# Kernel optimization log

Hardware: AMD Instinct MI355X
Metric: run time of the kernel (lower is better)

## Reference

```python
import jax, jax.numpy as jnp
import numpy as np

N_NODES = 100000

def gcn_conv(x, W, b, row, col, n_nodes):
    """PyG-style GCNConv: add self-loops, symmetric deg normalization,
    linear transform, scatter-add aggregation over edges, plus bias."""
    h = x @ W  # [N, out]
    loop = jnp.arange(n_nodes, dtype=row.dtype)
    r = jnp.concatenate([row, loop])  # source nodes
    c = jnp.concatenate([col, loop])  # target nodes
    w = jnp.ones(r.shape[0], dtype=x.dtype)  # edge_weight=None -> ones (incl. self-loop fill=1)
    deg = jax.ops.segment_sum(w, c, num_segments=n_nodes)
    dinv = jnp.where(deg > 0, jax.lax.rsqrt(deg), 0.0).astype(x.dtype)
    norm = dinv[r] * dinv[c]  # [E+N]
    msg = h[r] * norm[:, None]  # gather + scale, [E+N, out]
    out = jax.ops.segment_sum(msg, c, num_segments=n_nodes)
    return out + b


def setup_inputs() -> dict:
    key = jax.random.key(0)
    k0, k1, k2, k3, k4, k5 = jax.random.split(key, 6)
    F_in, H, C = 128, 64, 40
    E = 1_600_000
    x = jax.random.normal(k0, (N_NODES, F_in), dtype=jnp.float32)
    edge_index = jax.random.randint(k1, (2, E), 0, N_NODES, dtype=jnp.int64 if jax.config.jax_enable_x64 else jnp.int32)
    # Glorot init like torch Linear
    s1 = 1.0 / np.sqrt(F_in)
    s2 = 1.0 / np.sqrt(H)
    W1 = jax.random.uniform(k2, (F_in, H), jnp.float32, -s1, s1)
    b1 = jax.random.uniform(k3, (H,), jnp.float32, -s1, s1)
    W2 = jax.random.uniform(k4, (H, C), jnp.float32, -s2, s2)
    b2 = jax.random.uniform(k5, (C,), jnp.float32, -s2, s2)
    return {"x": x, "edge_index": edge_index, "W1": W1, "b1": b1, "W2": W2, "b2": b2}


def reference(x, edge_index, W1, b1, W2, b2):
    row, col = edge_index[0], edge_index[1]
    # eval mode: dropout(p=0.5, training=False) is identity
    h = gcn_conv(x, W1, b1, row, col, N_NODES)
    h = jax.nn.relu(h)
    out = gcn_conv(h, W2, b2, row, col, N_NODES)
    return out
```

## Files before the change

kernel.cpp:

```cpp
#include <hip/hip_runtime.h>
#include <hip/hip_fp16.h>


#define FIN 128
#define H1  64
#define C2  40
#define GP  40
#define TILE 8192
#define BCAP 7168
#define WTS 132
#define W2TS 68

typedef _Float16 half4_t __attribute__((ext_vector_type(4)));
typedef float float4_t __attribute__((ext_vector_type(4)));

__global__ __launch_bounds__(256) void k_wprep(const float* __restrict__ W1,
                                               _Float16* __restrict__ W1th,
                                               _Float16* __restrict__ W1tl,
                                               const float* __restrict__ W2,
                                               _Float16* __restrict__ W2th,
                                               _Float16* __restrict__ W2tl) {
    int idx = blockIdx.x * 256 + threadIdx.x;
    if (idx < FIN * H1) {
        int k = idx >> 6, o = idx & 63;
        float wv = W1[k * H1 + o];
        _Float16 hi = (_Float16)wv;
        W1th[o * WTS + k] = hi;
        W1tl[o * WTS + k] = (_Float16)(wv - (float)hi);
    } else if (idx < FIN * H1 + 48 * 64) {
        int i = idx - FIN * H1;
        int kk = i / 48, n = i % 48;
        float wv = (n < C2) ? W2[kk * C2 + n] : 0.f;
        _Float16 hi = (_Float16)wv;
        W2th[n * W2TS + kk] = hi;
        W2tl[n * W2TS + kk] = (_Float16)(wv - (float)hi);
    }
}

__global__ __launch_bounds__(256) void k_hist(const int* __restrict__ col, int E,
                                              int* __restrict__ bucketCnt, int NB) {
    __shared__ int lh[512];
    int t = threadIdx.x;
    for (int i = t; i < NB; i += 256) lh[i] = 0;
    __syncthreads();
    int base = blockIdx.x * TILE;
    int cnt = min(TILE, E - base);
    for (int i = t; i < cnt; i += 256) atomicAdd(&lh[col[base + i] >> 8], 1);
    __syncthreads();
    for (int b = t; b < NB; b += 256) if (lh[b]) atomicAdd(&bucketCnt[b], lh[b]);
}

__global__ __launch_bounds__(512) void k_scan(const int* __restrict__ bucketCnt,
                                              int* __restrict__ rawBase,
                                              int* __restrict__ padBase,
                                              int* __restrict__ gcursor,
                                              __half* __restrict__ h1,
                                              __half* __restrict__ g,
                                              int NB, int N) {
    __shared__ int sr[512], sp[512];
    int t = threadIdx.x;
    int c = (t < NB) ? bucketCnt[t] : 0;
    int p = (t < NB) ? (((c + 7) & ~7) + 2048) : 0;
    sr[t] = c; sp[t] = p;
    __syncthreads();
    for (int off = 1; off < 512; off <<= 1) {
        int a = (t >= off) ? sr[t - off] : 0;
        int b = (t >= off) ? sp[t - off] : 0;
        __syncthreads();
        sr[t] += a; sp[t] += b;
        __syncthreads();
    }
    if (t <= NB) {
        rawBase[t] = sr[t] - ((t < NB) ? c : 0);
        padBase[t] = sp[t] - ((t < NB) ? p : 0);
        if (t < NB) gcursor[t] = sr[t] - c;
    }
    if (t < 32) ((unsigned*)(h1 + (size_t)N * H1))[t] = 0u;
    else if (t < 52) ((unsigned*)(g + (size_t)N * GP))[t - 32] = 0u;
}

__global__ __launch_bounds__(512) void k_scatter(const int* __restrict__ row,
                                                 const int* __restrict__ col,
                                                 int* __restrict__ gcursor,
                                                 int* __restrict__ pairs,
                                                 int E, int NB) {
    __shared__ int2 stage[TILE];
    __shared__ int lcnt[512];
    __shared__ int lex[512];
    __shared__ int gbase[512];
    int t = threadIdx.x, tile = blockIdx.x;
    int base = tile * TILE;
    int cnt = min(TILE, E - base);

    lcnt[t] = 0;
    __syncthreads();
    for (int i = t; i < cnt; i += 512) atomicAdd(&lcnt[col[base + i] >> 8], 1);
    __syncthreads();

    int myc = lcnt[t];
    lex[t] = myc;
    __syncthreads();
    for (int off = 1; off < 512; off <<= 1) {
        int u = (t >= off) ? lex[t - off] : 0;
        __syncthreads();
        lex[t] += u;
        __syncthreads();
    }
    int ex = lex[t] - myc;
    __syncthreads();
    lex[t] = ex;
    lcnt[t] = ex;
    if (t < NB && myc > 0) gbase[t] = atomicAdd(&gcursor[t], myc);
    __syncthreads();

    for (int i = t; i < cnt; i += 512) {
        int r = row[base + i], c = col[base + i];
        int lpos = atomicAdd(&lcnt[c >> 8], 1);
        stage[lpos] = make_int2(r, c);
    }
    __syncthreads();

    for (int i = t; i < cnt; i += 512) {
        int2 p = stage[i];
        int b = p.y >> 8;
        pairs[gbase[b] + (i - lex[b])] = p.x | ((p.y & 255) << 24);
    }
}

__global__ __launch_bounds__(512) void k_bucket(const int* __restrict__ pairs,
                                                const int* __restrict__ rawBase,
                                                const int* __restrict__ padBase,
                                                int* __restrict__ rowptr,
                                                int* __restrict__ deg,
                                                int* __restrict__ esrc,
                                                int N, int NB) {
    __shared__ int dcnt[256];
    __shared__ int sr[256], sp[256];
    __shared__ int cur[256];
    __shared__ int outbuf[BCAP];
    int t = threadIdx.x, b = blockIdx.x;
    int d0 = b << 8;
    int nd = min(256, N - d0);
    int bstart = rawBase[b];
    int cnt = rawBase[b + 1] - bstart;
    int pstart = padBase[b];

    if (t < 256) dcnt[t] = 0;
    __syncthreads();
    for (int i = t; i < cnt; i += 512) {
        unsigned p = (unsigned)pairs[bstart + i];
        atomicAdd(&dcnt[p >> 24], 1);
    }
    __syncthreads();

    int myc = 0, myp = 0;
    if (t < 256) {
        myc = dcnt[t];
        myp = (myc + 7) & ~7;
        sr[t] = myc; sp[t] = myp;
    }
    __syncthreads();
    for (int off = 1; off < 256; off <<= 1) {
        int a = 0, c2 = 0;
        if (t < 256 && t >= off) { a = sr[t - off]; c2 = sp[t - off]; }
        __syncthreads();
        if (t < 256) { sr[t] += a; sp[t] += c2; }
        __syncthreads();
    }
    if (t < 256) {
        int pex = sp[t] - myp;
        cur[t] = pex;
        if (t < nd) {
            rowptr[d0 + t] = pstart + pex;
            deg[d0 + t] = myc;
        }
    }
    __syncthreads();
    int pcnt = sp[255];

    if (pcnt <= BCAP) {
        for (int i = t; i < cnt; i += 512) {
            unsigned p = (unsigned)pairs[bstart + i];
            int lpos = atomicAdd(&cur[p >> 24], 1);
            outbuf[lpos] = (int)(p & 0xFFFFFF);
        }
        __syncthreads();
        if (t < 256) {
            int pex = sp[t] - myp;
            for (int j = myc; j < myp; ++j) outbuf[pex + j] = N;
        }
        __syncthreads();
        for (int i = t; i < pcnt; i += 512) esrc[pstart + i] = outbuf[i];
    } else {
        for (int i = t; i < cnt; i += 512) {
            unsigned p = (unsigned)pairs[bstart + i];
            int lpos = atomicAdd(&cur[p >> 24], 1);
            esrc[pstart + lpos] = (int)(p & 0xFFFFFF);
        }
        __syncthreads();
        if (t < 256) {
            int pex = sp[t] - myp;
            for (int j = myc; j < myp; ++j) esrc[pstart + pex + j] = N;
        }
    }
}

__global__ __launch_bounds__(256) void k_gemm1m(const float* __restrict__ x,
                                                const _Float16* __restrict__ W1th,
                                                const _Float16* __restrict__ W1tl,
                                                const int* __restrict__ deg,
                                                __half* __restrict__ h1, int N) {
    __shared__ alignas(16) _Float16 Wh[H1 * WTS];
    __shared__ alignas(16) _Float16 Wl[H1 * WTS];
    int t = threadIdx.x;

    {
        const uint4* sh = (const uint4*)W1th;
        const uint4* sl = (const uint4*)W1tl;
        uint4* dh = (uint4*)Wh;
        uint4* dl = (uint4*)Wl;
        for (int i = t; i < (H1 * WTS) / 8; i += 256) { dh[i] = sh[i]; dl[i] = sl[i]; }
    }

    int wv = t >> 6, l = t & 63;
    int col = l & 15;
    int krow = l >> 4;
    int node = blockIdx.x * 64 + wv * 16 + col;
    int nodec = min(node, N - 1);

    half4_t bh[8], bl[8];
    const float4* xr = (const float4*)(x + (size_t)nodec * FIN);
#pragma unroll
    for (int kt = 0; kt < 8; ++kt) {
        float4 v = xr[kt * 4 + krow];
        half4_t hi, lo;
        hi[0] = (_Float16)v.x; lo[0] = (_Float16)(v.x - (float)hi[0]);
        hi[1] = (_Float16)v.y; lo[1] = (_Float16)(v.y - (float)hi[1]);
        hi[2] = (_Float16)v.z; lo[2] = (_Float16)(v.z - (float)hi[2]);
        hi[3] = (_Float16)v.w; lo[3] = (_Float16)(v.w - (float)hi[3]);
        bh[kt] = hi; bl[kt] = lo;
    }
    float dcv = rsqrtf((float)deg[nodec] + 1.0f);
    __syncthreads();

    float4_t acc[4];
#pragma unroll
    for (int ot = 0; ot < 4; ++ot) acc[ot] = (float4_t){0.f, 0.f, 0.f, 0.f};

#pragma unroll
    for (int kt = 0; kt < 8; ++kt) {
#pragma unroll
        for (int ot = 0; ot < 4; ++ot) {
            int aoff = ((ot * 16 + col) * WTS + kt * 16 + krow * 4) >> 2;
            half4_t ah = ((const half4_t*)Wh)[aoff];
            half4_t al = ((const half4_t*)Wl)[aoff];
            acc[ot] = __builtin_amdgcn_mfma_f32_16x16x16f16(ah, bh[kt], acc[ot], 0, 0, 0);
            acc[ot] = __builtin_amdgcn_mfma_f32_16x16x16f16(ah, bl[kt], acc[ot], 0, 0, 0);
            acc[ot] = __builtin_amdgcn_mfma_f32_16x16x16f16(al, bh[kt], acc[ot], 0, 0, 0);
        }
    }

    if (node < N) {
#pragma unroll
        for (int ot = 0; ot < 4; ++ot) {
            union { __half h[4]; uint2 u; } pk;
#pragma unroll
            for (int r = 0; r < 4; ++r) pk.h[r] = __float2half_rn(acc[ot][r] * dcv);
            *(uint2*)&h1[(size_t)node * H1 + ot * 16 + krow * 4] = pk.u;
        }
    }
}

__global__ __launch_bounds__(512) void k_agg1mm(const int* __restrict__ rowptr,
                                                const int* __restrict__ deg,
                                                const int* __restrict__ esrc,
                                                const __half* __restrict__ h1,
                                                const float* __restrict__ b1,
                                                const _Float16* __restrict__ W2th,
                                                const _Float16* __restrict__ W2tl,
                                                __half* __restrict__ g, int N) {
    __shared__ alignas(16) _Float16 hsh[64][W2TS];
    __shared__ alignas(16) _Float16 hsl[64][W2TS];
    __shared__ alignas(16) _Float16 Wth[48][W2TS];
    __shared__ alignas(16) _Float16 Wtl[48][W2TS];
    __shared__ float sdc[64];
    int t = threadIdx.x;
    int node0 = blockIdx.x * 64;

    {
        const uint4* sh = (const uint4*)W2th;
        const uint4* sl = (const uint4*)W2tl;
        uint4* dh = (uint4*)Wth;
        uint4* dl = (uint4*)Wtl;
        for (int i = t; i < (48 * W2TS) / 8; i += 512) { dh[i] = sh[i]; dl[i] = sl[i]; }
    }

    int wv = t >> 6, lane = t & 63;
    int half = lane >> 5;
    int f = lane & 31;
    float2 b1v = *(const float2*)&b1[2 * f];
    const __half2* hp = (const __half2*)h1;

#pragma unroll 1
    for (int j = 0; j < 8; ++j) {
        int r = wv * 8 + j;
        int node = node0 + r;
        if (node >= N) {
            if (lane < 32) { *(unsigned*)&hsh[r][2 * f] = 0u; *(unsigned*)&hsl[r][2 * f] = 0u; }
            if (lane == 0) sdc[r] = 0.f;
            continue;
        }
        int start = rowptr[node], d = deg[node];
        int d8 = (d + 7) & ~7;
        float dc = rsqrtf((float)d + 1.0f);
        float ax = 0.f, ay = 0.f;
        int i = 0;
        int4 sA = *(const int4*)&esrc[start + half * 8];
        int4 sB = *(const int4*)&esrc[start + half * 8 + 4];
#pragma unroll 1
        for (; i + 16 <= d8; i += 16) {
            int4 cA = sA, cB = sB;
            int nb = start + i + 16 + half * 8;
            sA = *(const int4*)&esrc[nb];
            sB = *(const int4*)&esrc[nb + 4];
            float2 v0 = __half22float2(hp[cA.x * 32 + f]);
            float2 v1 = __half22float2(hp[cA.y * 32 + f]);
            float2 v2 = __half22float2(hp[cA.z * 32 + f]);
            float2 v3 = __half22float2(hp[cA.w * 32 + f]);
            float2 v4 = __half22float2(hp[cB.x * 32 + f]);
            float2 v5 = __half22float2(hp[cB.y * 32 + f]);
            float2 v6 = __half22float2(hp[cB.z * 32 + f]);
            float2 v7 = __half22float2(hp[cB.w * 32 + f]);
            ax += ((v0.x + v1.x) + (v2.x + v3.x)) + ((v4.x + v5.x) + (v6.x + v7.x));
            ay += ((v0.y + v1.y) + (v2.y + v3.y)) + ((v4.y + v5.y) + (v6.y + v7.y));
        }
        if (i < d8) {
            int4 s = *(const int4*)&esrc[start + i + half * 4];
            float2 v0 = __half22float2(hp[s.x * 32 + f]);
            float2 v1 = __half22float2(hp[s.y * 32 + f]);
            float2 v2 = __half22float2(hp[s.z * 32 + f]);
            float2 v3 = __half22float2(hp[s.w * 32 + f]);
            ax += (v0.x + v1.x) + (v2.x + v3.x);
            ay += (v0.y + v1.y) + (v2.y + v3.y);
        }
        ax += __shfl(ax, lane ^ 32);
        ay += __shfl(ay, lane ^ 32);
        float2 sv = __half22float2(hp[node * 32 + f]);
        ax = fmaxf(fmaf(dc, ax + sv.x, b1v.x), 0.f);
        ay = fmaxf(fmaf(dc, ay + sv.y, b1v.y), 0.f);
        if (lane < 32) {
            _Float16 axh = (_Float16)ax;
            _Float16 ayh = (_Float16)ay;
            _Float16 axl = (_Float16)(ax - (float)axh);
            _Float16 ayl = (_Float16)(ay - (float)ayh);
            union { _Float16 h[2]; unsigned u; } ph, pl;
            ph.h[0] = axh; ph.h[1] = ayh;
            pl.h[0] = axl; pl.h[1] = ayl;
            *(unsigned*)&hsh[r][2 * f] = ph.u;
            *(unsigned*)&hsl[r][2 * f] = pl.u;
        }
        if (lane == 0) sdc[r] = dc;
    }
    __syncthreads();

    int l15 = lane & 15, kg = (lane >> 4) * 4;
#pragma unroll 1
    for (int tile = wv; tile < 12; tile += 8) {
        int mt = tile & 3, nt = tile >> 2;
        int arow = mt * 16 + l15;
        int bcol = nt * 16 + l15;
        float4_t acc = (float4_t){0.f, 0.f, 0.f, 0.f};
#pragma unroll
        for (int kt = 0; kt < 4; ++kt) {
            int ko = kt * 16 + kg;
            half4_t ah = *(const half4_t*)&hsh[arow][ko];
            half4_t al = *(const half4_t*)&hsl[arow][ko];
            half4_t bh = *(const half4_t*)&Wth[bcol][ko];
            half4_t bl = *(const half4_t*)&Wtl[bcol][ko];
            acc = __builtin_amdgcn_mfma_f32_16x16x16f16(ah, bh, acc, 0, 0, 0);
            acc = __builtin_amdgcn_mfma_f32_16x16x16f16(ah, bl, acc, 0, 0, 0);
            acc = __builtin_amdgcn_mfma_f32_16x16x16f16(al, bh, acc, 0, 0, 0);
        }
        int colo = nt * 16 + l15;
        if (colo < C2) {
#pragma unroll
            for (int r2 = 0; r2 < 4; ++r2) {
                int nd = mt * 16 + (lane >> 4) * 4 + r2;
                int node = node0 + nd;
                if (node < N) {
                    g[(size_t)node * GP + colo] = __float2half_rn(acc[r2] * sdc[nd]);
                }
            }
        }
    }
}

__global__ __launch_bounds__(256) void k_agg2(const int* __restrict__ rowptr,
                                              const int* __restrict__ deg,
                                              const int* __restrict__ esrc,
                                              const __half* __restrict__ g,
                                              const float* __restrict__ b2,
                                              float* __restrict__ out, int N) {
    int w = (int)((blockIdx.x * blockDim.x + threadIdx.x) >> 6);
    int lane = threadIdx.x & 63;
    if (w >= N) return;
    int half = lane >> 5;
    int f = lane & 31;
    bool act = f < 20;
    const __half2* gp = (const __half2*)g;

    int start = rowptr[w], d = deg[w];
    int d8 = (d + 7) & ~7;
    float dc = rsqrtf((float)d + 1.0f);
    float ax = 0.f, ay = 0.f;
    if (act) {
        int i = 0;
        int4 sA = *(const int4*)&esrc[start + half * 8];
        int4 sB = *(const int4*)&esrc[start + half * 8 + 4];
#pragma unroll 1
        for (; i + 16 <= d8; i += 16) {
            int4 cA = sA, cB = sB;
            int nb = start + i + 16 + half * 8;
            sA = *(const int4*)&esrc[nb];
            sB = *(const int4*)&esrc[nb + 4];
            float2 v0 = __half22float2(gp[cA.x * 20 + f]);
            float2 v1 = __half22float2(gp[cA.y * 20 + f]);
            float2 v2 = __half22float2(gp[cA.z * 20 + f]);
            float2 v3 = __half22float2(gp[cA.w * 20 + f]);
            float2 v4 = __half22float2(gp[cB.x * 20 + f]);
            float2 v5 = __half22float2(gp[cB.y * 20 + f]);
            float2 v6 = __half22float2(gp[cB.z * 20 + f]);
            float2 v7 = __half22float2(gp[cB.w * 20 + f]);
            ax += ((v0.x + v1.x) + (v2.x + v3.x)) + ((v4.x + v5.x) + (v6.x + v7.x));
            ay += ((v0.y + v1.y) + (v2.y + v3.y)) + ((v4.y + v5.y) + (v6.y + v7.y));
        }
        if (i < d8) {
            int4 s = *(const int4*)&esrc[start + i + half * 4];
            float2 v0 = __half22float2(gp[s.x * 20 + f]);
            float2 v1 = __half22float2(gp[s.y * 20 + f]);
            float2 v2 = __half22float2(gp[s.z * 20 + f]);
            float2 v3 = __half22float2(gp[s.w * 20 + f]);
            ax += (v0.x + v1.x) + (v2.x + v3.x);
            ay += (v0.y + v1.y) + (v2.y + v3.y);
        }
    }
    ax += __shfl(ax, lane ^ 32);
    ay += __shfl(ay, lane ^ 32);
    if (lane < 32 && act) {
        float2 b2v = *(const float2*)&b2[2 * f];
        float2 sv = __half22float2(gp[w * 20 + f]);
        float2 o;
        o.x = fmaf(dc, ax + sv.x, b2v.x);
        o.y = fmaf(dc, ay + sv.y, b2v.y);
        *(float2*)&out[(size_t)w * C2 + 2 * f] = o;
    }
}

extern "C" void kernel_launch(void* const* d_in, const int* in_sizes, int n_in,
                              void* d_out, int out_size, void* d_ws, size_t ws_size,
                              hipStream_t stream) {
    const float* x   = (const float*)d_in[0];
    const int*   ei  = (const int*)d_in[1];
    const float* W1  = (const float*)d_in[2];
    const float* b1  = (const float*)d_in[3];
    const float* W2  = (const float*)d_in[4];
    const float* b2  = (const float*)d_in[5];
    float* out = (float*)d_out;

    const int N = in_sizes[0] / FIN;
    const int E = in_sizes[1] / 2;
    const int* row = ei;
    const int* col = ei + E;

    const int NB = (N + 255) >> 8;
    const int T  = (E + TILE - 1) / TILE;
    const int EP = E + NB * 2048 + 8192;

    char* ws = (char*)d_ws;
    size_t off = 0;
    int*    bucketCnt = (int*)(ws + off);    off += (size_t)NB * 4;
    int*    rawBase   = (int*)(ws + off);    off += (size_t)(NB + 1) * 4;
    int*    padBase   = (int*)(ws + off);    off += (size_t)(NB + 1) * 4;
    int*    gcursor   = (int*)(ws + off);    off += (size_t)NB * 4;
    int*    deg       = (int*)(ws + off);    off += (size_t)N * 4;
    int*    rowptr    = (int*)(ws + off);    off += (size_t)N * 4;
    int*    pairs     = (int*)(ws + off);    off += (size_t)E * 4;
    off = (off + 15) & ~(size_t)15;
    int*    esrc      = (int*)(ws + off);    off += (size_t)EP * 4;
    off = (off + 15) & ~(size_t)15;
    _Float16* W1th    = (_Float16*)(ws + off); off += (size_t)H1 * WTS * 2;
    off = (off + 15) & ~(size_t)15;
    _Float16* W1tl    = (_Float16*)(ws + off); off += (size_t)H1 * WTS * 2;
    off = (off + 15) & ~(size_t)15;
    _Float16* W2th    = (_Float16*)(ws + off); off += (size_t)48 * W2TS * 2;
    off = (off + 15) & ~(size_t)15;
    _Float16* W2tl    = (_Float16*)(ws + off); off += (size_t)48 * W2TS * 2;
    off = (off + 15) & ~(size_t)15;
    __half* h1        = (__half*)(ws + off); off += (size_t)(N + 1) * H1 * 2;
    off = (off + 15) & ~(size_t)15;
    __half* g         = (__half*)(ws + off); off += (size_t)(N + 1) * GP * 2;

    hipMemsetAsync(bucketCnt, 0, (size_t)NB * 4, stream);

    int gblocks = (N + 63) / 64;

    k_wprep<<<(FIN * H1 + 48 * 64 + 255) / 256, 256, 0, stream>>>(W1, W1th, W1tl, W2, W2th, W2tl);

    k_hist<<<T, 256, 0, stream>>>(col, E, bucketCnt, NB);
    k_scan<<<1, 512, 0, stream>>>(bucketCnt, rawBase, padBase, gcursor, h1, g, NB, N);
    k_scatter<<<T, 512, 0, stream>>>(row, col, gcursor, pairs, E, NB);
    k_bucket<<<NB, 512, 0, stream>>>(pairs, rawBase, padBase, rowptr, deg, esrc, N, NB);

    k_gemm1m<<<gblocks, 256, 0, stream>>>(x, W1th, W1tl, deg, h1, N);

    k_agg1mm<<<gblocks, 512, 0, stream>>>(rowptr, deg, esrc, h1, b1, W2th, W2tl, g, N);

    k_agg2<<<((size_t)N * 64 + 255) / 256, 256, 0, stream>>>(rowptr, deg, esrc, g, b2, out, N);
}
```

Before: 238.4 us.

## Fuse layer-1 GEMM into bucket kernel and fold memset into weight prep

Merges the first-layer MFMA GEMM into the per-bucket CSR build kernel, so each 256-node bucket block also computes h1 for its nodes using degrees already held in shared memory. The separate GEMM launch and the global deg reread go away. The memset of the bucket counters moves into the weight-prep kernel, and the aggregation kernel stages rowptr and deg in shared memory. The cost is much more shared memory per bucket block (outbuf plus two W1 tiles), which lowers occupancy. Each block now also runs the GEMM for 256 nodes with 8 waves doing 2 tiles each, so there is less GEMM parallelism.

```diff
diff --git a/kernel.cpp b/kernel.cpp
--- a/kernel.cpp
+++ b/kernel.cpp
@@ -19,8 +19,10 @@
                                                _Float16* __restrict__ W1tl,
                                                const float* __restrict__ W2,
                                                _Float16* __restrict__ W2th,
-                                               _Float16* __restrict__ W2tl) {
+                                               _Float16* __restrict__ W2tl,
+                                               int* __restrict__ bucketCnt, int NB) {
     int idx = blockIdx.x * 256 + threadIdx.x;
+    if (idx < NB) bucketCnt[idx] = 0;
     if (idx < FIN * H1) {
         int k = idx >> 6, o = idx & 63;
         float wv = W1[k * H1 + o];
@@ -133,11 +135,18 @@
                                                 int* __restrict__ rowptr,
                                                 int* __restrict__ deg,
                                                 int* __restrict__ esrc,
+                                                const float* __restrict__ x,
+                                                const _Float16* __restrict__ W1th,
+                                                const _Float16* __restrict__ W1tl,
+                                                __half* __restrict__ h1,
                                                 int N, int NB) {
     __shared__ int dcnt[256];
     __shared__ int sr[256], sp[256];
     __shared__ int cur[256];
     __shared__ int outbuf[BCAP];
+    __shared__ alignas(16) _Float16 Wh[H1 * WTS];
+    __shared__ alignas(16) _Float16 Wl[H1 * WTS];
+    __shared__ float sdc[256];
     int t = threadIdx.x, b = blockIdx.x;
     int d0 = b << 8;
     int nd = min(256, N - d0);
@@ -145,6 +154,14 @@
     int cnt = rawBase[b + 1] - bstart;
     int pstart = padBase[b];
 
+    {
+        const uint4* shp = (const uint4*)W1th;
+        const uint4* slp = (const uint4*)W1tl;
+        uint4* dh = (uint4*)Wh;
+        uint4* dl = (uint4*)Wl;
+        for (int i = t; i < (H1 * WTS) / 8; i += 512) { dh[i] = shp[i]; dl[i] = slp[i]; }
+    }
+
     if (t < 256) dcnt[t] = 0;
     __syncthreads();
     for (int i = t; i < cnt; i += 512) {
@@ -170,6 +187,7 @@
     if (t < 256) {
         int pex = sp[t] - myp;
         cur[t] = pex;
+        sdc[t] = (t < nd) ? rsqrtf((float)myc + 1.0f) : 0.f;
         if (t < nd) {
             rowptr[d0 + t] = pstart + pex;
             deg[d0 + t] = myc;
@@ -203,70 +221,56 @@
             for (int j = myc; j < myp; ++j) esrc[pstart + pex + j] = N;
         }
     }
-}
-
-__global__ __launch_bounds__(256) void k_gemm1m(const float* __restrict__ x,
-                                                const _Float16* __restrict__ W1th,
-                                                const _Float16* __restrict__ W1tl,
-                                                const int* __restrict__ deg,
-                                                __half* __restrict__ h1, int N) {
-    __shared__ alignas(16) _Float16 Wh[H1 * WTS];
-    __shared__ alignas(16) _Float16 Wl[H1 * WTS];
-    int t = threadIdx.x;
-
-    {
-        const uint4* sh = (const uint4*)W1th;
-        const uint4* sl = (const uint4*)W1tl;
-        uint4* dh = (uint4*)Wh;
-        uint4* dl = (uint4*)Wl;
-        for (int i = t; i < (H1 * WTS) / 8; i += 256) { dh[i] = sh[i]; dl[i] = sl[i]; }
-    }
+    __syncthreads();
 
     int wv = t >> 6, l = t & 63;
     int col = l & 15;
     int krow = l >> 4;
-    int node = blockIdx.x * 64 + wv * 16 + col;
-    int nodec = min(node, N - 1);
-
-    half4_t bh[8], bl[8];
-    const float4* xr = (const float4*)(x + (size_t)nodec * FIN);
-#pragma unroll
-    for (int kt = 0; kt < 8; ++kt) {
-        float4 v = xr[kt * 4 + krow];
-        half4_t hi, lo;
-        hi[0] = (_Float16)v.x; lo[0] = (_Float16)(v.x - (float)hi[0]);
-        hi[1] = (_Float16)v.y; lo[1] = (_Float16)(v.y - (float)hi[1]);
-        hi[2] = (_Float16)v.z; lo[2] = (_Float16)(v.z - (float)hi[2]);
-        hi[3] = (_Float16)v.w; lo[3] = (_Float16)(v.w - (float)hi[3]);
-        bh[kt] = hi; bl[kt] = lo;
-    }
-    float dcv = rsqrtf((float)deg[nodec] + 1.0f);
-    __syncthreads();
-
-    float4_t acc[4];
-#pragma unroll
-    for (int ot = 0; ot < 4; ++ot) acc[ot] = (float4_t){0.f, 0.f, 0.f, 0.f};
-
-#pragma unroll
-    for (int kt = 0; kt < 8; ++kt) {
-#pragma unroll
-        for (int ot = 0; ot < 4; ++ot) {
-            int aoff = ((ot * 16 + col) * WTS + kt * 16 + krow * 4) >> 2;
-            half4_t ah = ((const half4_t*)Wh)[aoff];
-            half4_t al = ((const half4_t*)Wl)[aoff];
-            acc[ot] = __builtin_amdgcn_mfma_f32_16x16x16f16(ah, bh[kt], acc[ot], 0, 0, 0);
-            acc[ot] = __builtin_amdgcn_mfma_f32_16x16x16f16(ah, bl[kt], acc[ot], 0, 0, 0);
-            acc[ot] = __builtin_amdgcn_mfma_f32_16x16x16f16(al, bh[kt], acc[ot], 0, 0, 0);
-        }
-    }
-
-    if (node < N) {
-#pragma unroll
-        for (int ot = 0; ot < 4; ++ot) {
-            union { __half h[4]; uint2 u; } pk;
-#pragma unroll
-            for (int r = 0; r < 4; ++r) pk.h[r] = __float2half_rn(acc[ot][r] * dcv);
-            *(uint2*)&h1[(size_t)node * H1 + ot * 16 + krow * 4] = pk.u;
+#pragma unroll 1
+    for (int tt = 0; tt < 2; ++tt) {
+        int nodeIdx = (wv * 2 + tt) * 16 + col;
+        int node = d0 + nodeIdx;
+        int nodec = min(node, N - 1);
+
+        half4_t bh[8], bl[8];
+        const float4* xr = (const float4*)(x + (size_t)nodec * FIN);
+#pragma unroll
+        for (int kt = 0; kt < 8; ++kt) {
+            float4 v = xr[kt * 4 + krow];
+            half4_t hi, lo;
+            hi[0] = (_Float16)v.x; lo[0] = (_Float16)(v.x - (float)hi[0]);
+            hi[1] = (_Float16)v.y; lo[1] = (_Float16)(v.y - (float)hi[1]);
+            hi[2] = (_Float16)v.z; lo[2] = (_Float16)(v.z - (float)hi[2]);
+            hi[3] = (_Float16)v.w; lo[3] = (_Float16)(v.w - (float)hi[3]);
+            bh[kt] = hi; bl[kt] = lo;
+        }
+        float dcv = sdc[nodeIdx];
+
+        float4_t acc[4];
+#pragma unroll
+        for (int ot = 0; ot < 4; ++ot) acc[ot] = (float4_t){0.f, 0.f, 0.f, 0.f};
+
+#pragma unroll
+        for (int kt = 0; kt < 8; ++kt) {
+#pragma unroll
+            for (int ot = 0; ot < 4; ++ot) {
+                int aoff = ((ot * 16 + col) * WTS + kt * 16 + krow * 4) >> 2;
+                half4_t ah = ((const half4_t*)Wh)[aoff];
+                half4_t al = ((const half4_t*)Wl)[aoff];
+                acc[ot] = __builtin_amdgcn_mfma_f32_16x16x16f16(ah, bh[kt], acc[ot], 0, 0, 0);
+                acc[ot] = __builtin_amdgcn_mfma_f32_16x16x16f16(ah, bl[kt], acc[ot], 0, 0, 0);
+                acc[ot] = __builtin_amdgcn_mfma_f32_16x16x16f16(al, bh[kt], acc[ot], 0, 0, 0);
+            }
+        }
+
+        if (node < N) {
+#pragma unroll
+            for (int ot = 0; ot < 4; ++ot) {
+                union { __half h[4]; uint2 u; } pk;
+#pragma unroll
+                for (int r = 0; r < 4; ++r) pk.h[r] = __float2half_rn(acc[ot][r] * dcv);
+                *(uint2*)&h1[(size_t)node * H1 + ot * 16 + krow * 4] = pk.u;
+            }
         }
     }
 }
@@ -284,6 +288,7 @@
     __shared__ alignas(16) _Float16 Wth[48][W2TS];
     __shared__ alignas(16) _Float16 Wtl[48][W2TS];
     __shared__ float sdc[64];
+    __shared__ int srp[64], sdg[64];
     int t = threadIdx.x;
     int node0 = blockIdx.x * 64;
 
@@ -294,6 +299,12 @@
         uint4* dl = (uint4*)Wtl;
         for (int i = t; i < (48 * W2TS) / 8; i += 512) { dh[i] = sh[i]; dl[i] = sl[i]; }
     }
+    if (t < 64) {
+        int node = node0 + t;
+        srp[t] = (node < N) ? rowptr[node] : 0;
+        sdg[t] = (node < N) ? deg[node] : 0;
+    }
+    __syncthreads();
 
     int wv = t >> 6, lane = t & 63;
     int half = lane >> 5;
@@ -310,7 +321,7 @@
             if (lane == 0) sdc[r] = 0.f;
             continue;
         }
-        int start = rowptr[node], d = deg[node];
+        int start = srp[r], d = sdg[r];
         int d8 = (d + 7) & ~7;
         float dc = rsqrtf((float)d + 1.0f);
         float ax = 0.f, ay = 0.f;
@@ -500,18 +511,16 @@
     off = (off + 15) & ~(size_t)15;
     __half* g         = (__half*)(ws + off); off += (size_t)(N + 1) * GP * 2;
 
-    hipMemsetAsync(bucketCnt, 0, (size_t)NB * 4, stream);
-
     int gblocks = (N + 63) / 64;
 
-    k_wprep<<<(FIN * H1 + 48 * 64 + 255) / 256, 256, 0, stream>>>(W1, W1th, W1tl, W2, W2th, W2tl);
+    k_wprep<<<(FIN * H1 + 48 * 64 + 255) / 256, 256, 0, stream>>>(
+        W1, W1th, W1tl, W2, W2th, W2tl, bucketCnt, NB);
 
     k_hist<<<T, 256, 0, stream>>>(col, E, bucketCnt, NB);
     k_scan<<<1, 512, 0, stream>>>(bucketCnt, rawBase, padBase, gcursor, h1, g, NB, N);
     k_scatter<<<T, 512, 0, stream>>>(row, col, gcursor, pairs, E, NB);
-    k_bucket<<<NB, 512, 0, stream>>>(pairs, rawBase, padBase, rowptr, deg, esrc, N, NB);
-
-    k_gemm1m<<<gblocks, 256, 0, stream>>>(x, W1th, W1tl, deg, h1, N);
+    k_bucket<<<NB, 512, 0, stream>>>(pairs, rawBase, padBase, rowptr, deg, esrc,
+                                     x, W1th, W1tl, h1, N, NB);
 
     k_agg1mm<<<gblocks, 512, 0, stream>>>(rowptr, deg, esrc, h1, b1, W2th, W2tl, g, N);
 
```

New measurement: 240.3 us. About the same (+0.8%).

## Remove scan kernel and memset by recomputing bucket prefix sums inside consumers

Applied to the files above, without the earlier changes.

The separate single-block scan kernel and the memset of bucket counters are removed. Zeroing of counters and padding rows moves into the weight-prep kernel, and each scatter and bucket block recomputes the 512-entry prefix sum over bucket counts itself. Scatter now takes offsets from a per-bucket atomic cursor, the bucket kernel stages its pairs in shared memory before its two passes over them, and the aggregation kernel preloads rowptr and degree for its 64 nodes into shared memory. This saves two launches and a serial dependency, but adds redundant scan work and extra shared memory in every block, which can lower occupancy.

```diff
diff --git a/kernel.cpp b/kernel.cpp
--- a/kernel.cpp
+++ b/kernel.cpp
@@ -8,6 +8,7 @@
 #define GP  40
 #define TILE 8192
 #define BCAP 7168
+#define STAGE_CAP 4608
 #define WTS 132
 #define W2TS 68
 
@@ -19,8 +20,14 @@
                                                _Float16* __restrict__ W1tl,
                                                const float* __restrict__ W2,
                                                _Float16* __restrict__ W2th,
-                                               _Float16* __restrict__ W2tl) {
+                                               _Float16* __restrict__ W2tl,
+                                               int* __restrict__ bucketCnt,
+                                               int* __restrict__ goff,
+                                               __half* __restrict__ h1,
+                                               __half* __restrict__ g,
+                                               int NB, int N) {
     int idx = blockIdx.x * 256 + threadIdx.x;
+    if (idx < NB) { bucketCnt[idx] = 0; goff[idx] = 0; }
     if (idx < FIN * H1) {
         int k = idx >> 6, o = idx & 63;
         float wv = W1[k * H1 + o];
@@ -34,6 +41,10 @@
         _Float16 hi = (_Float16)wv;
         W2th[n * W2TS + kk] = hi;
         W2tl[n * W2TS + kk] = (_Float16)(wv - (float)hi);
+    } else if (idx < FIN * H1 + 48 * 64 + 32) {
+        ((unsigned*)(h1 + (size_t)N * H1))[idx - (FIN * H1 + 48 * 64)] = 0u;
+    } else if (idx < FIN * H1 + 48 * 64 + 52) {
+        ((unsigned*)(g + (size_t)N * GP))[idx - (FIN * H1 + 48 * 64 + 32)] = 0u;
     }
 }
 
@@ -50,48 +61,32 @@
     for (int b = t; b < NB; b += 256) if (lh[b]) atomicAdd(&bucketCnt[b], lh[b]);
 }
 
-__global__ __launch_bounds__(512) void k_scan(const int* __restrict__ bucketCnt,
-                                              int* __restrict__ rawBase,
-                                              int* __restrict__ padBase,
-                                              int* __restrict__ gcursor,
-                                              __half* __restrict__ h1,
-                                              __half* __restrict__ g,
-                                              int NB, int N) {
-    __shared__ int sr[512], sp[512];
-    int t = threadIdx.x;
-    int c = (t < NB) ? bucketCnt[t] : 0;
-    int p = (t < NB) ? (((c + 7) & ~7) + 2048) : 0;
-    sr[t] = c; sp[t] = p;
-    __syncthreads();
-    for (int off = 1; off < 512; off <<= 1) {
-        int a = (t >= off) ? sr[t - off] : 0;
-        int b = (t >= off) ? sp[t - off] : 0;
-        __syncthreads();
-        sr[t] += a; sp[t] += b;
-        __syncthreads();
-    }
-    if (t <= NB) {
-        rawBase[t] = sr[t] - ((t < NB) ? c : 0);
-        padBase[t] = sp[t] - ((t < NB) ? p : 0);
-        if (t < NB) gcursor[t] = sr[t] - c;
-    }
-    if (t < 32) ((unsigned*)(h1 + (size_t)N * H1))[t] = 0u;
-    else if (t < 52) ((unsigned*)(g + (size_t)N * GP))[t - 32] = 0u;
-}
-
 __global__ __launch_bounds__(512) void k_scatter(const int* __restrict__ row,
                                                  const int* __restrict__ col,
-                                                 int* __restrict__ gcursor,
+                                                 const int* __restrict__ bucketCnt,
+                                                 int* __restrict__ goff,
                                                  int* __restrict__ pairs,
                                                  int E, int NB) {
     __shared__ int2 stage[TILE];
     __shared__ int lcnt[512];
     __shared__ int lex[512];
     __shared__ int gbase[512];
+    __shared__ int scs[512];
     int t = threadIdx.x, tile = blockIdx.x;
     int base = tile * TILE;
     int cnt = min(TILE, E - base);
 
+    int bc = (t < NB) ? bucketCnt[t] : 0;
+    scs[t] = bc;
+    __syncthreads();
+    for (int off = 1; off < 512; off <<= 1) {
+        int u = (t >= off) ? scs[t - off] : 0;
+        __syncthreads();
+        scs[t] += u;
+        __syncthreads();
+    }
+    int rex = scs[t] - bc;
+
     lcnt[t] = 0;
     __syncthreads();
     for (int i = t; i < cnt; i += 512) atomicAdd(&lcnt[col[base + i] >> 8], 1);
@@ -110,7 +105,7 @@
     __syncthreads();
     lex[t] = ex;
     lcnt[t] = ex;
-    if (t < NB && myc > 0) gbase[t] = atomicAdd(&gcursor[t], myc);
+    if (t < NB && myc > 0) gbase[t] = rex + atomicAdd(&goff[t], myc);
     __syncthreads();
 
     for (int i = t; i < cnt; i += 512) {
@@ -128,8 +123,7 @@
 }
 
 __global__ __launch_bounds__(512) void k_bucket(const int* __restrict__ pairs,
-                                                const int* __restrict__ rawBase,
-                                                const int* __restrict__ padBase,
+                                                const int* __restrict__ bucketCnt,
                                                 int* __restrict__ rowptr,
                                                 int* __restrict__ deg,
                                                 int* __restrict__ esrc,
@@ -137,18 +131,39 @@
     __shared__ int dcnt[256];
     __shared__ int sr[256], sp[256];
     __shared__ int cur[256];
+    __shared__ int bsc[512], bsp[512];
+    __shared__ int sb[4];
     __shared__ int outbuf[BCAP];
+    __shared__ int pstage[STAGE_CAP];
     int t = threadIdx.x, b = blockIdx.x;
     int d0 = b << 8;
     int nd = min(256, N - d0);
-    int bstart = rawBase[b];
-    int cnt = rawBase[b + 1] - bstart;
-    int pstart = padBase[b];
-
+
+    int c0 = (t < NB) ? bucketCnt[t] : 0;
+    int p0 = (t < NB) ? (((c0 + 7) & ~7) + 2048) : 0;
+    bsc[t] = c0; bsp[t] = p0;
+    __syncthreads();
+    for (int off = 1; off < 512; off <<= 1) {
+        int a = (t >= off) ? bsc[t - off] : 0;
+        int bb = (t >= off) ? bsp[t - off] : 0;
+        __syncthreads();
+        bsc[t] += a; bsp[t] += bb;
+        __syncthreads();
+    }
+    if (t == b) { sb[0] = bsc[b] - c0; sb[1] = c0; sb[2] = bsp[b] - p0; }
+    __syncthreads();
+    int bstart = sb[0];
+    int cnt = sb[1];
+    int pstart = sb[2];
+
+    bool staged = (cnt <= STAGE_CAP);
+    if (staged) {
+        for (int i = t; i < cnt; i += 512) pstage[i] = pairs[bstart + i];
+    }
     if (t < 256) dcnt[t] = 0;
     __syncthreads();
     for (int i = t; i < cnt; i += 512) {
-        unsigned p = (unsigned)pairs[bstart + i];
+        unsigned p = (unsigned)(staged ? pstage[i] : pairs[bstart + i]);
         atomicAdd(&dcnt[p >> 24], 1);
     }
     __syncthreads();
@@ -180,7 +195,7 @@
 
     if (pcnt <= BCAP) {
         for (int i = t; i < cnt; i += 512) {
-            unsigned p = (unsigned)pairs[bstart + i];
+            unsigned p = (unsigned)(staged ? pstage[i] : pairs[bstart + i]);
             int lpos = atomicAdd(&cur[p >> 24], 1);
             outbuf[lpos] = (int)(p & 0xFFFFFF);
         }
@@ -193,7 +208,7 @@
         for (int i = t; i < pcnt; i += 512) esrc[pstart + i] = outbuf[i];
     } else {
         for (int i = t; i < cnt; i += 512) {
-            unsigned p = (unsigned)pairs[bstart + i];
+            unsigned p = (unsigned)(staged ? pstage[i] : pairs[bstart + i]);
             int lpos = atomicAdd(&cur[p >> 24], 1);
             esrc[pstart + lpos] = (int)(p & 0xFFFFFF);
         }
@@ -284,6 +299,7 @@
     __shared__ alignas(16) _Float16 Wth[48][W2TS];
     __shared__ alignas(16) _Float16 Wtl[48][W2TS];
     __shared__ float sdc[64];
+    __shared__ int srp[64], sdg[64];
     int t = threadIdx.x;
     int node0 = blockIdx.x * 64;
 
@@ -294,6 +310,12 @@
         uint4* dl = (uint4*)Wtl;
         for (int i = t; i < (48 * W2TS) / 8; i += 512) { dh[i] = sh[i]; dl[i] = sl[i]; }
     }
+    if (t < 64) {
+        int node = node0 + t;
+        srp[t] = (node < N) ? rowptr[node] : 0;
+        sdg[t] = (node < N) ? deg[node] : 0;
+    }
+    __syncthreads();
 
     int wv = t >> 6, lane = t & 63;
     int half = lane >> 5;
@@ -310,7 +332,7 @@
             if (lane == 0) sdc[r] = 0.f;
             continue;
         }
-        int start = rowptr[node], d = deg[node];
+        int start = srp[r], d = sdg[r];
         int d8 = (d + 7) & ~7;
         float dc = rsqrtf((float)d + 1.0f);
         float ax = 0.f, ay = 0.f;
@@ -479,9 +501,7 @@
     char* ws = (char*)d_ws;
     size_t off = 0;
     int*    bucketCnt = (int*)(ws + off);    off += (size_t)NB * 4;
-    int*    rawBase   = (int*)(ws + off);    off += (size_t)(NB + 1) * 4;
-    int*    padBase   = (int*)(ws + off);    off += (size_t)(NB + 1) * 4;
-    int*    gcursor   = (int*)(ws + off);    off += (size_t)NB * 4;
+    int*    goff      = (int*)(ws + off);    off += (size_t)NB * 4;
     int*    deg       = (int*)(ws + off);    off += (size_t)N * 4;
     int*    rowptr    = (int*)(ws + off);    off += (size_t)N * 4;
     int*    pairs     = (int*)(ws + off);    off += (size_t)E * 4;
@@ -500,16 +520,14 @@
     off = (off + 15) & ~(size_t)15;
     __half* g         = (__half*)(ws + off); off += (size_t)(N + 1) * GP * 2;
 
-    hipMemsetAsync(bucketCnt, 0, (size_t)NB * 4, stream);
-
     int gblocks = (N + 63) / 64;
 
-    k_wprep<<<(FIN * H1 + 48 * 64 + 255) / 256, 256, 0, stream>>>(W1, W1th, W1tl, W2, W2th, W2tl);
+    k_wprep<<<(FIN * H1 + 48 * 64 + 52 + 255) / 256, 256, 0, stream>>>(
+        W1, W1th, W1tl, W2, W2th, W2tl, bucketCnt, goff, h1, g, NB, N);
 
     k_hist<<<T, 256, 0, stream>>>(col, E, bucketCnt, NB);
-    k_scan<<<1, 512, 0, stream>>>(bucketCnt, rawBase, padBase, gcursor, h1, g, NB, N);
-    k_scatter<<<T, 512, 0, stream>>>(row, col, gcursor, pairs, E, NB);
-    k_bucket<<<NB, 512, 0, stream>>>(pairs, rawBase, padBase, rowptr, deg, esrc, N, NB);
+    k_scatter<<<T, 512, 0, stream>>>(row, col, bucketCnt, goff, pairs, E, NB);
+    k_bucket<<<NB, 512, 0, stream>>>(pairs, bucketCnt, rowptr, deg, esrc, N, NB);
 
     k_gemm1m<<<gblocks, 256, 0, stream>>>(x, W1th, W1tl, deg, h1, N);
 
```

Result: no change. 241.9 us (+1.5%).
